# Kernel optimization log

Measured on AMD Instinct MI355X. Metric: run time of the kernel, lower is better.

Reference implementation:

```python
import jax, jax.numpy as jnp
import numpy as np

T, E, IN, OUT, A, R = 16384, 8, 1024, 1024, 8, 16  # tokens, experts, d_in, d_out, adapters, lora rank


def prepare_routing(x, indices, num_groups):
    """Sort tokens by group index; return sorted x, per-group counts, unsort map, sorted ids."""
    sort_idx = jnp.argsort(indices)  # stable sort keeps within-group order
    x_sorted = x[sort_idx]
    group_sizes = jnp.bincount(indices, length=num_groups).astype(jnp.int32)
    unsort_indices = jnp.argsort(sort_idx)
    return x_sorted, group_sizes, unsort_indices, indices[sort_idx]


def setup_inputs() -> dict:
    key = jax.random.key(0)
    ks = jax.random.split(key, 6)
    # tokens pre-sorted by expert: group_sizes must sum to T exactly
    expert_ids = jnp.sort(jax.random.randint(ks[0], (T,), 0, E))
    group_sizes = jnp.bincount(expert_ids, length=E).astype(jnp.int32)
    x = jax.random.normal(ks[1], (T, IN), jnp.float32)
    adapter_indices_sorted = jax.random.randint(ks[2], (T,), 0, A)
    weight = jax.random.normal(ks[3], (E, IN, OUT), jnp.float32) * 0.02
    lora_A = jax.random.normal(ks[4], (A, E, IN, R), jnp.float32) * 0.02
    lora_B = jax.random.normal(ks[5], (A, E, R, OUT), jnp.float32) * 0.02
    lora_scaling = jnp.ones((A,), jnp.float32)
    return {
        "x": x,
        "group_sizes": group_sizes,
        "adapter_indices_sorted": adapter_indices_sorted,
        "weight": weight,
        "lora_A": lora_A,
        "lora_B": lora_B,
        "lora_scaling": lora_scaling,
    }


def reference(x, group_sizes, adapter_indices_sorted, weight, lora_A, lora_B, lora_scaling):
    # base grouped GEMM over experts: [T,IN] x [E,IN,OUT] -> [T,OUT]
    base_out = jax.lax.ragged_dot(x, weight, group_sizes)

    # per-token expert id from contiguous group sizes
    expert_ids = jnp.repeat(jnp.arange(E), group_sizes, total_repeat_length=T)
    flattened = expert_ids * A + adapter_indices_sorted  # expert-major (E,A) group id

    # flatten adapters x experts into E*A groups (expert-major to match flattened ids)
    A_mat = lora_A.transpose(1, 0, 2, 3).reshape(E * A, IN, R)
    B_mat = lora_B.transpose(1, 0, 2, 3).reshape(E * A, R, OUT)

    x_sorted, combined_gs, unsort_indices, _ = prepare_routing(x, flattened, E * A)
    inter = jax.lax.ragged_dot(x_sorted, A_mat, combined_gs)          # [T,R]
    lora_out_sorted = jax.lax.ragged_dot(inter, B_mat, combined_gs)   # [T,OUT]
    lora_out = lora_out_sorted[unsort_indices]
    lora_out = lora_out * lora_scaling[adapter_indices_sorted][:, None]
    return base_out + lora_out
```

## Files before the change

### kernel.cpp

```cpp
#include <hip/hip_runtime.h>

#define T_TOK 16384
#define NEXP 8
#define DIN 1024
#define DOUT 1024
#define NADP 8
#define RANK 16
#define NGRP 64
#define MAXP1 520
#define BK 32
#define NKSTEP 32

typedef float f32x4 __attribute__((ext_vector_type(4)));
typedef float f32x16 __attribute__((ext_vector_type(16)));
typedef __bf16 bf16x8 __attribute__((ext_vector_type(8)));

typedef __attribute__((address_space(3))) void lds_void;
typedef __attribute__((address_space(1))) void g_void;

static __device__ __forceinline__ unsigned short f2bf(float f) {
    union { float f; unsigned u; } c; c.f = f;
    unsigned r = c.u + 0x7FFFu + ((c.u >> 16) & 1u);
    return (unsigned short)(r >> 16);
}

#define XB2 2048
#define NBW 2048
__global__ __launch_bounds__(256) void k_convert_all(const float* __restrict__ x,
                                                     const float* __restrict__ W,
                                                     const float* __restrict__ lA,
                                                     const float* __restrict__ lB,
                                                     unsigned short* __restrict__ xb,
                                                     unsigned short* __restrict__ Wt,
                                                     unsigned short* __restrict__ Agt,
                                                     unsigned short* __restrict__ Blt) {
    __shared__ __attribute__((aligned(16))) unsigned short lds_u[16 * 1032];
    int b = blockIdx.x;
    int t = threadIdx.x;
    if (b < XB2) {
        const size_t total = (size_t)(T_TOK + 128) * DIN / 4;
        const size_t conv  = (size_t)T_TOK * DIN / 4;
        size_t gid = (size_t)b * 256 + t;
#pragma unroll
        for (int it = 0; it < 9; it++) {
            size_t u = gid + (size_t)it * (XB2 * 256);
            if (u < total) {
                ushort4 o;
                if (u < conv) {
                    float4 v = *(const float4*)(x + u * 4);
                    o.x = f2bf(v.x); o.y = f2bf(v.y); o.z = f2bf(v.z); o.w = f2bf(v.w);
                } else {
                    o.x = 0; o.y = 0; o.z = 0; o.w = 0;
                }
                *(ushort4*)(xb + u * 4) = o;
            }
        }
    } else if (b < XB2 + NBW) {
        int idx = b - XB2;
        int e = idx >> 8;
        int k0 = ((idx >> 4) & 15) * 64, n0 = (idx & 15) * 64;
        const float* We = W + (size_t)e * DIN * DOUT;
        unsigned short* Wte = Wt + (size_t)e * DIN * DOUT;
        unsigned* lds32 = (unsigned*)lds_u;
        int kp = t >> 3;
        int nc = (t & 7) * 8;
        const float* r0 = We + (size_t)(k0 + 2 * kp) * DOUT + n0 + nc;
        const float* r1 = r0 + DOUT;
        float4 a0 = *(const float4*)r0, a1 = *(const float4*)(r0 + 4);
        float4 c0 = *(const float4*)r1, c1 = *(const float4*)(r1 + 4);
        lds32[(nc + 0) * 34 + kp] = (unsigned)f2bf(a0.x) | ((unsigned)f2bf(c0.x) << 16);
        lds32[(nc + 1) * 34 + kp] = (unsigned)f2bf(a0.y) | ((unsigned)f2bf(c0.y) << 16);
        lds32[(nc + 2) * 34 + kp] = (unsigned)f2bf(a0.z) | ((unsigned)f2bf(c0.z) << 16);
        lds32[(nc + 3) * 34 + kp] = (unsigned)f2bf(a0.w) | ((unsigned)f2bf(c0.w) << 16);
        lds32[(nc + 4) * 34 + kp] = (unsigned)f2bf(a1.x) | ((unsigned)f2bf(c1.x) << 16);
        lds32[(nc + 5) * 34 + kp] = (unsigned)f2bf(a1.y) | ((unsigned)f2bf(c1.y) << 16);
        lds32[(nc + 6) * 34 + kp] = (unsigned)f2bf(a1.z) | ((unsigned)f2bf(c1.z) << 16);
        lds32[(nc + 7) * 34 + kp] = (unsigned)f2bf(a1.w) | ((unsigned)f2bf(c1.w) << 16);
        __syncthreads();
        int n = t >> 2, kq = (t & 3) * 8;
        uint2 d0 = *(const uint2*)&lds32[n * 34 + kq + 0];
        uint2 d1 = *(const uint2*)&lds32[n * 34 + kq + 2];
        uint2 d2 = *(const uint2*)&lds32[n * 34 + kq + 4];
        uint2 d3 = *(const uint2*)&lds32[n * 34 + kq + 6];
        uint4 v0; v0.x = d0.x; v0.y = d0.y; v0.z = d1.x; v0.w = d1.y;
        uint4 v1; v1.x = d2.x; v1.y = d2.y; v1.z = d3.x; v1.w = d3.y;
        *(uint4*)(Wte + (size_t)(n0 + n) * DIN + k0 + kq * 2) = v0;
        *(uint4*)(Wte + (size_t)(n0 + n) * DIN + k0 + kq * 2 + 8) = v1;
    } else if (b < XB2 + NBW + NGRP) {
        int g = b - (XB2 + NBW);
        int a = g & 7, e = g >> 3;
        const float* src = lA + (size_t)(a * NEXP + e) * DIN * RANK;
#pragma unroll
        for (int it = 0; it < 4; it++) {
            int k = it * 256 + t;
            const float4* p = (const float4*)(src + (size_t)k * RANK);
            float4 v0 = p[0], v1 = p[1], v2 = p[2], v3 = p[3];
            lds_u[0 * 1032 + k] = f2bf(v0.x);  lds_u[1 * 1032 + k] = f2bf(v0.y);
            lds_u[2 * 1032 + k] = f2bf(v0.z);  lds_u[3 * 1032 + k] = f2bf(v0.w);
            lds_u[4 * 1032 + k] = f2bf(v1.x);  lds_u[5 * 1032 + k] = f2bf(v1.y);
            lds_u[6 * 1032 + k] = f2bf(v1.z);  lds_u[7 * 1032 + k] = f2bf(v1.w);
            lds_u[8 * 1032 + k] = f2bf(v2.x);  lds_u[9 * 1032 + k] = f2bf(v2.y);
            lds_u[10 * 1032 + k] = f2bf(v2.z); lds_u[11 * 1032 + k] = f2bf(v2.w);
            lds_u[12 * 1032 + k] = f2bf(v3.x); lds_u[13 * 1032 + k] = f2bf(v3.y);
            lds_u[14 * 1032 + k] = f2bf(v3.z); lds_u[15 * 1032 + k] = f2bf(v3.w);
        }
        __syncthreads();
        unsigned short* dst = Agt + (size_t)g * RANK * DIN;
        int r = t >> 4, ks = (t & 15) * 64;
#pragma unroll
        for (int j = 0; j < 8; j++)
            *(uint4*)(dst + r * DIN + ks + j * 8) = *(const uint4*)&lds_u[r * 1032 + ks + j * 8];
    } else {
        int idx = b - (XB2 + NBW + NGRP);
        int e = idx >> 3, nc = idx & 7;
        int k = t >> 1, half = t & 1;
        int a = k >> 4, r = k & 15;
        const float* src = lB + ((size_t)(a * NEXP + e) * RANK + r) * DOUT + nc * 128 + half * 64;
#pragma unroll
        for (int j = 0; j < 16; j++) {
            float4 v = *(const float4*)(src + j * 4);
            int nl = half * 64 + j * 4;
            lds_u[k * 129 + nl + 0] = f2bf(v.x);
            lds_u[k * 129 + nl + 1] = f2bf(v.y);
            lds_u[k * 129 + nl + 2] = f2bf(v.z);
            lds_u[k * 129 + nl + 3] = f2bf(v.w);
        }
        __syncthreads();
        int nl = t >> 1, kh = t & 1;
        unsigned short* dst = Blt + ((size_t)(e * 1024 + nc * 128 + nl)) * 128 + kh * 64;
#pragma unroll
        for (int g2 = 0; g2 < 8; g2++) {
            uint4 pv;
            unsigned short s0 = lds_u[(kh * 64 + g2 * 8 + 0) * 129 + nl];
            unsigned short s1 = lds_u[(kh * 64 + g2 * 8 + 1) * 129 + nl];
            unsigned short s2 = lds_u[(kh * 64 + g2 * 8 + 2) * 129 + nl];
            unsigned short s3 = lds_u[(kh * 64 + g2 * 8 + 3) * 129 + nl];
            unsigned short s4 = lds_u[(kh * 64 + g2 * 8 + 4) * 129 + nl];
            unsigned short s5 = lds_u[(kh * 64 + g2 * 8 + 5) * 129 + nl];
            unsigned short s6 = lds_u[(kh * 64 + g2 * 8 + 6) * 129 + nl];
            unsigned short s7 = lds_u[(kh * 64 + g2 * 8 + 7) * 129 + nl];
            pv.x = (unsigned)s0 | ((unsigned)s1 << 16);
            pv.y = (unsigned)s2 | ((unsigned)s3 << 16);
            pv.z = (unsigned)s4 | ((unsigned)s5 << 16);
            pv.w = (unsigned)s6 | ((unsigned)s7 << 16);
            *(uint4*)(dst + g2 * 8) = pv;
        }
    }
}

__global__ __launch_bounds__(256) void k_pass1(const unsigned short* __restrict__ xb,
                                               const unsigned short* __restrict__ Agt,
                                               const int* __restrict__ gs,
                                               const int* __restrict__ aidx,
                                               const float* __restrict__ scal,
                                               unsigned short* __restrict__ interb) {
    int bid = blockIdx.x;
    int e = -1, m0 = 0, valid = 0;
    {
        int acc_t = 0, base = 0;
#pragma unroll
        for (int ee = 0; ee < NEXP; ee++) {
            int sz = gs[ee];
            int nt = (sz + 31) >> 5;
            if (e < 0 && bid < acc_t + nt) {
                int loc = bid - acc_t;
                e = ee; m0 = base + (loc << 5);
                int v = sz - (loc << 5); valid = v > 32 ? 32 : v;
            }
            acc_t += nt; base += sz;
        }
    }
    if (e < 0) return;

    int t = threadIdx.x;
    int lane = t & 63, w = t >> 6;
    int ln = lane & 15, q = lane >> 4;

    const unsigned short* A0 = Agt + ((size_t)(e * NADP + 2 * w) * RANK + ln) * DIN + q * 8;
    const unsigned short* A1 = A0 + (size_t)RANK * DIN;
    const unsigned short* X0 = xb + (size_t)(m0 + ln) * DIN + q * 8;

    f32x4 acc[2][2];
#pragma unroll
    for (int i = 0; i < 2; i++) {
        acc[i][0] = (f32x4){0.f, 0.f, 0.f, 0.f};
        acc[i][1] = (f32x4){0.f, 0.f, 0.f, 0.f};
    }

#pragma unroll 4
    for (int k0 = 0; k0 < DIN; k0 += 32) {
        bf16x8 b0 = *(const bf16x8*)(A0 + k0);
        bf16x8 b1 = *(const bf16x8*)(A1 + k0);
#pragma unroll
        for (int rg = 0; rg < 2; rg++) {
            bf16x8 af = *(const bf16x8*)(X0 + (size_t)(rg * 16) * DIN + k0);
            acc[rg][0] = __builtin_amdgcn_mfma_f32_16x16x32_bf16(b0, af, acc[rg][0], 0, 0, 0);
            acc[rg][1] = __builtin_amdgcn_mfma_f32_16x16x32_bf16(b1, af, acc[rg][1], 0, 0, 0);
        }
    }

    float s0 = scal[2 * w], s1 = scal[2 * w + 1];
#pragma unroll
    for (int rg = 0; rg < 2; rg++) {
        int tr = rg * 16 + ln;
        if (tr < valid) {
            int tok = m0 + tr;
            int a = aidx[tok];
            if (a == 2 * w) {
                f32x4 v = acc[rg][0];
                ushort4 u;
                u.x = f2bf(s0 * v[0]); u.y = f2bf(s0 * v[1]);
                u.z = f2bf(s0 * v[2]); u.w = f2bf(s0 * v[3]);
                *(ushort4*)(interb + (size_t)tok * RANK + q * 4) = u;
            } else if (a == 2 * w + 1) {
                f32x4 v = acc[rg][1];
                ushort4 u;
                u.x = f2bf(s1 * v[0]); u.y = f2bf(s1 * v[1]);
                u.z = f2bf(s1 * v[2]); u.w = f2bf(s1 * v[3]);
                *(ushort4*)(interb + (size_t)tok * RANK + q * 4) = u;
            }
        }
    }
}

__global__ __launch_bounds__(256) void k_gemm(const unsigned short* __restrict__ xb,
                                              const unsigned short* __restrict__ wt,
                                              const int* __restrict__ gs,
                                              const unsigned short* __restrict__ interb,
                                              const int* __restrict__ aidx,
                                              const unsigned short* __restrict__ Blt,
                                              float* __restrict__ out) {
    __shared__ __attribute__((aligned(16))) unsigned short smem[32768];

    int id = blockIdx.y * 8 + blockIdx.x;
    int xcd = id & 7;
    int j = id >> 3;
    int tileid = xcd * 17 + (j >> 3);
    int n0 = (j & 7) * 128;

    int e = -1, m0 = 0, valid = 0;
    {
        int acc_t = 0, base = 0;
#pragma unroll
        for (int ee = 0; ee < NEXP; ee++) {
            int sz = gs[ee];
            int nt = (sz + 127) >> 7;
            if (e < 0 && tileid < acc_t + nt) {
                int loc = tileid - acc_t;
                e = ee; m0 = base + (loc << 7);
                int v = sz - (loc << 7); valid = v > 128 ? 128 : v;
            }
            acc_t += nt; base += sz;
        }
    }
    if (e < 0) return;

    int t = threadIdx.x;
    int lane = t & 63;
    int wave = t >> 6;
    int wm = wave >> 1, wn = wave & 1;
    int r32 = lane & 31, hi = lane >> 5;

    const unsigned short* wte = wt + (size_t)e * DIN * DOUT;

    f32x16 acc[2][2];
#pragma unroll
    for (int i = 0; i < 2; i++)
#pragma unroll
        for (int j2 = 0; j2 < 2; j2++) acc[i][j2] = (f32x16)(0.f);

    int srow = wave * 16 + (lane >> 2);
    int skoff = (((lane & 3) ^ ((lane >> 2) ^ (lane >> 4)) ) & 3) * 8;
    const unsigned short* gA = xb + (size_t)m0 * DIN;
    const unsigned short* gB = wte + (size_t)n0 * DIN;

    auto STAGE = [&](int buf, int k0) {
#pragma unroll
        for (int jj = 0; jj < 2; jj++) {
            int row = jj * 64 + srow;
            __builtin_amdgcn_global_load_lds(
                (const g_void*)(gA + (size_t)row * DIN + k0 + skoff),
                (lds_void*)((char*)smem + buf * 16384 + jj * 4096 + wave * 1024), 16, 0, 0);
            __builtin_amdgcn_global_load_lds(
                (const g_void*)(gB + (size_t)row * DIN + k0 + skoff),
                (lds_void*)((char*)smem + buf * 16384 + 8192 + jj * 4096 + wave * 1024), 16, 0, 0);
        }
    };

    int fr = (r32 ^ (r32 >> 2)) & 3;

    auto COMPUTE = [&](int buf) {
        const char* Ab = (const char*)smem + buf * 16384;
        const char* Bb = Ab + 8192;
        __builtin_amdgcn_s_setprio(1);
#pragma unroll
        for (int kf = 0; kf < 2; kf++) {
            int kc = kf * 2 + hi;
            int slot = (kc ^ fr) * 16;
            bf16x8 af[2], bfr[2];
#pragma unroll
            for (int mi = 0; mi < 2; mi++) {
                int row = wm * 64 + mi * 32 + r32;
                af[mi] = *(const bf16x8*)(Ab + row * 64 + slot);
            }
#pragma unroll
            for (int ni = 0; ni < 2; ni++) {
                int row = wn * 64 + ni * 32 + r32;
                bfr[ni] = *(const bf16x8*)(Bb + row * 64 + slot);
            }
#pragma unroll
            for (int mi = 0; mi < 2; mi++)
#pragma unroll
                for (int ni = 0; ni < 2; ni++)
                    acc[mi][ni] = __builtin_amdgcn_mfma_f32_32x32x16_bf16(af[mi], bfr[ni], acc[mi][ni], 0, 0, 0);
        }
        __builtin_amdgcn_s_setprio(0);
    };

    STAGE(0, 0);
    STAGE(1, 32);
    STAGE(2, 64);
#pragma unroll
    for (int ts = 0; ts < NKSTEP; ts++) {
        if (ts < NKSTEP - 2)      asm volatile("s_waitcnt vmcnt(8)" ::: "memory");
        else if (ts == NKSTEP - 2) asm volatile("s_waitcnt vmcnt(4)" ::: "memory");
        else                       asm volatile("s_waitcnt vmcnt(0)" ::: "memory");
        __builtin_amdgcn_s_barrier();
        COMPUTE(ts & 3);
        if (ts < NKSTEP - 3) {
            __builtin_amdgcn_s_barrier();
            STAGE((ts + 3) & 3, (ts + 3) * BK);
        }
    }

    {
        int row = t >> 1, h = t & 1;
        int rs = row & 15;
        uint4 z = {0u, 0u, 0u, 0u};
        uint4 payload = z;
        int pslot = -1;
        if (row < valid) {
            int tok = m0 + row;
            int a = aidx[tok];
            payload = *(const uint4*)(interb + (size_t)tok * RANK + h * 8);
            pslot = a * 2 + h;
        }
#pragma unroll
        for (int l2 = 0; l2 < 8; l2++) {
            int l = l2 * 2 + h;
            int phys = l ^ rs;
            *(uint4*)((char*)smem + row * 256 + phys * 16) = (l == pslot) ? payload : z;
        }
    }
    __syncthreads();
#pragma unroll
    for (int kf = 0; kf < 8; kf++) {
        int kc = kf * 2 + hi;
        bf16x8 af[2], bfr[2];
#pragma unroll
        for (int ni = 0; ni < 2; ni++) {
            int n = wn * 64 + ni * 32 + r32;
            bfr[ni] = *(const bf16x8*)(Blt + ((size_t)(e * 1024 + n0 + n)) * 128 + kc * 8);
        }
#pragma unroll
        for (int mi = 0; mi < 2; mi++) {
            int row = wm * 64 + mi * 32 + r32;
            int slot = kc ^ (r32 & 15);
            af[mi] = *(const bf16x8*)((const char*)smem + row * 256 + slot * 16);
        }
#pragma unroll
        for (int mi = 0; mi < 2; mi++)
#pragma unroll
            for (int ni = 0; ni < 2; ni++)
                acc[mi][ni] = __builtin_amdgcn_mfma_f32_32x32x16_bf16(af[mi], bfr[ni], acc[mi][ni], 0, 0, 0);
    }

#pragma unroll
    for (int mi = 0; mi < 2; mi++) {
#pragma unroll
        for (int r = 0; r < 16; r++) {
            int row32 = (r & 3) + 8 * (r >> 2) + 4 * hi;
            int row_l = wm * 64 + mi * 32 + row32;
            if (row_l < valid) {
                float* orow = out + (size_t)(m0 + row_l) * DOUT + n0 + wn * 64 + r32;
#pragma unroll
                for (int ni = 0; ni < 2; ni++)
                    orow[ni * 32] = acc[mi][ni][r];
            }
        }
    }
}

extern "C" void kernel_launch(void* const* d_in, const int* in_sizes, int n_in,
                              void* d_out, int out_size, void* d_ws, size_t ws_size,
                              hipStream_t stream) {
    (void)in_sizes; (void)n_in; (void)out_size; (void)ws_size;
    const float* x    = (const float*)d_in[0];
    const int*   gs   = (const int*)d_in[1];
    const int*   aidx = (const int*)d_in[2];
    const float* W    = (const float*)d_in[3];
    const float* lA   = (const float*)d_in[4];
    const float* lB   = (const float*)d_in[5];
    const float* scal = (const float*)d_in[6];
    float* out = (float*)d_out;

    char* ws = (char*)d_ws;
    unsigned short* xb     = (unsigned short*)ws;        size_t o = 33816576;
    unsigned short* wt     = (unsigned short*)(ws + o);  o += 16777216;
    unsigned short* Agt    = (unsigned short*)(ws + o);  o += 2097152;
    unsigned short* Blt    = (unsigned short*)(ws + o);  o += 2097152;
    unsigned short* interb = (unsigned short*)(ws + o);  o += 524288;

    k_convert_all<<<XB2 + NBW + NGRP + 64, 256, 0, stream>>>(x, W, lA, lB, xb, wt, Agt, Blt);
    k_pass1<<<MAXP1, 256, 0, stream>>>(xb, Agt, gs, aidx, scal, interb);
    k_gemm<<<dim3(8, 136), 256, 0, stream>>>(xb, wt, gs, interb, aidx, Blt, out);
}
```

Measured before the change: 269.3 us.

## Fuse LoRA-A pass into conversion kernel and halve GEMM barriers per K-step

The LoRA-A projection pass now reads fp32 x directly and converts it on the fly. That lets it run as part of the conversion launch, concurrently with the x/W/B conversions, instead of waiting for the bf16 copy of x. Converting lora_A moves into a small separate kernel that runs first. The main GEMM now processes two 32-wide LDS buffers per iteration (BK 64, 16 steps), which halves the barrier and wait count. The trade-off is extra fp32 reads and conversion work in the LoRA pass, and less prefetch slack in the pipeline.

```diff
diff --git a/kernel.cpp b/kernel.cpp
--- a/kernel.cpp
+++ b/kernel.cpp
@@ -7,9 +7,9 @@
 #define NADP 8
 #define RANK 16
 #define NGRP 64
-#define MAXP1 520
-#define BK 32
-#define NKSTEP 32
+#define NP1 520
+#define BK 64
+#define NKSTEP 16
 
 typedef float f32x4 __attribute__((ext_vector_type(4)));
 typedef float f32x16 __attribute__((ext_vector_type(16)));
@@ -24,23 +24,131 @@
     return (unsigned short)(r >> 16);
 }
 
+__global__ __launch_bounds__(256) void k_prep(const float* __restrict__ lA,
+                                              unsigned short* __restrict__ Agt) {
+    __shared__ __attribute__((aligned(16))) unsigned short lds_u[16 * 1032];
+    int g = blockIdx.x;
+    int t = threadIdx.x;
+    int a = g & 7, e = g >> 3;
+    const float* src = lA + (size_t)(a * NEXP + e) * DIN * RANK;
+#pragma unroll
+    for (int it = 0; it < 4; it++) {
+        int k = it * 256 + t;
+        const float4* p = (const float4*)(src + (size_t)k * RANK);
+        float4 v0 = p[0], v1 = p[1], v2 = p[2], v3 = p[3];
+        lds_u[0 * 1032 + k] = f2bf(v0.x);  lds_u[1 * 1032 + k] = f2bf(v0.y);
+        lds_u[2 * 1032 + k] = f2bf(v0.z);  lds_u[3 * 1032 + k] = f2bf(v0.w);
+        lds_u[4 * 1032 + k] = f2bf(v1.x);  lds_u[5 * 1032 + k] = f2bf(v1.y);
+        lds_u[6 * 1032 + k] = f2bf(v1.z);  lds_u[7 * 1032 + k] = f2bf(v1.w);
+        lds_u[8 * 1032 + k] = f2bf(v2.x);  lds_u[9 * 1032 + k] = f2bf(v2.y);
+        lds_u[10 * 1032 + k] = f2bf(v2.z); lds_u[11 * 1032 + k] = f2bf(v2.w);
+        lds_u[12 * 1032 + k] = f2bf(v3.x); lds_u[13 * 1032 + k] = f2bf(v3.y);
+        lds_u[14 * 1032 + k] = f2bf(v3.z); lds_u[15 * 1032 + k] = f2bf(v3.w);
+    }
+    __syncthreads();
+    unsigned short* dst = Agt + (size_t)g * RANK * DIN;
+    int r = t >> 4, ks = (t & 15) * 64;
+#pragma unroll
+    for (int j = 0; j < 8; j++)
+        *(uint4*)(dst + r * DIN + ks + j * 8) = *(const uint4*)&lds_u[r * 1032 + ks + j * 8];
+}
+
 #define XB2 2048
 #define NBW 2048
-__global__ __launch_bounds__(256) void k_convert_all(const float* __restrict__ x,
-                                                     const float* __restrict__ W,
-                                                     const float* __restrict__ lA,
-                                                     const float* __restrict__ lB,
-                                                     unsigned short* __restrict__ xb,
-                                                     unsigned short* __restrict__ Wt,
-                                                     unsigned short* __restrict__ Agt,
-                                                     unsigned short* __restrict__ Blt) {
+__global__ __launch_bounds__(256) void k_mega(const float* __restrict__ x,
+                                              const float* __restrict__ W,
+                                              const float* __restrict__ lB,
+                                              const unsigned short* __restrict__ Agt,
+                                              const int* __restrict__ gs,
+                                              const int* __restrict__ aidx,
+                                              const float* __restrict__ scal,
+                                              unsigned short* __restrict__ xb,
+                                              unsigned short* __restrict__ Wt,
+                                              unsigned short* __restrict__ Blt,
+                                              unsigned short* __restrict__ interb) {
     __shared__ __attribute__((aligned(16))) unsigned short lds_u[16 * 1032];
     int b = blockIdx.x;
     int t = threadIdx.x;
-    if (b < XB2) {
+    if (b < NP1) {
+        int e = -1, m0 = 0, valid = 0;
+        {
+            int acc_t = 0, base = 0;
+#pragma unroll
+            for (int ee = 0; ee < NEXP; ee++) {
+                int sz = gs[ee];
+                int nt = (sz + 31) >> 5;
+                if (e < 0 && b < acc_t + nt) {
+                    int loc = b - acc_t;
+                    e = ee; m0 = base + (loc << 5);
+                    int v = sz - (loc << 5); valid = v > 32 ? 32 : v;
+                }
+                acc_t += nt; base += sz;
+            }
+        }
+        if (e < 0) return;
+
+        int lane = t & 63, w = t >> 6;
+        int ln = lane & 15, q = lane >> 4;
+
+        const unsigned short* A0 = Agt + ((size_t)(e * NADP + 2 * w) * RANK + ln) * DIN + q * 8;
+        const unsigned short* A1 = A0 + (size_t)RANK * DIN;
+        int r0 = m0 + ln;       if (r0 >= T_TOK) r0 = T_TOK - 1;
+        int r1 = m0 + 16 + ln;  if (r1 >= T_TOK) r1 = T_TOK - 1;
+        const float* X0 = x + (size_t)r0 * DIN + q * 8;
+        const float* X1 = x + (size_t)r1 * DIN + q * 8;
+
+        f32x4 acc[2][2];
+#pragma unroll
+        for (int i = 0; i < 2; i++) {
+            acc[i][0] = (f32x4){0.f, 0.f, 0.f, 0.f};
+            acc[i][1] = (f32x4){0.f, 0.f, 0.f, 0.f};
+        }
+
+#pragma unroll 4
+        for (int k0 = 0; k0 < DIN; k0 += 32) {
+            bf16x8 b0 = *(const bf16x8*)(A0 + k0);
+            bf16x8 b1 = *(const bf16x8*)(A1 + k0);
+#pragma unroll
+            for (int rg = 0; rg < 2; rg++) {
+                const float* xp = (rg == 0) ? (X0 + k0) : (X1 + k0);
+                float4 u0 = *(const float4*)xp;
+                float4 u1 = *(const float4*)(xp + 4);
+                unsigned short af_u[8];
+                af_u[0] = f2bf(u0.x); af_u[1] = f2bf(u0.y); af_u[2] = f2bf(u0.z); af_u[3] = f2bf(u0.w);
+                af_u[4] = f2bf(u1.x); af_u[5] = f2bf(u1.y); af_u[6] = f2bf(u1.z); af_u[7] = f2bf(u1.w);
+                bf16x8 af = *(const bf16x8*)af_u;
+                acc[rg][0] = __builtin_amdgcn_mfma_f32_16x16x32_bf16(b0, af, acc[rg][0], 0, 0, 0);
+                acc[rg][1] = __builtin_amdgcn_mfma_f32_16x16x32_bf16(b1, af, acc[rg][1], 0, 0, 0);
+            }
+        }
+
+        float s0 = scal[2 * w], s1 = scal[2 * w + 1];
+#pragma unroll
+        for (int rg = 0; rg < 2; rg++) {
+            int tr = rg * 16 + ln;
+            if (tr < valid) {
+                int tok = m0 + tr;
+                int a = aidx[tok];
+                if (a == 2 * w) {
+                    f32x4 v = acc[rg][0];
+                    ushort4 u;
+                    u.x = f2bf(s0 * v[0]); u.y = f2bf(s0 * v[1]);
+                    u.z = f2bf(s0 * v[2]); u.w = f2bf(s0 * v[3]);
+                    *(ushort4*)(interb + (size_t)tok * RANK + q * 4) = u;
+                } else if (a == 2 * w + 1) {
+                    f32x4 v = acc[rg][1];
+                    ushort4 u;
+                    u.x = f2bf(s1 * v[0]); u.y = f2bf(s1 * v[1]);
+                    u.z = f2bf(s1 * v[2]); u.w = f2bf(s1 * v[3]);
+                    *(ushort4*)(interb + (size_t)tok * RANK + q * 4) = u;
+                }
+            }
+        }
+    } else if (b < NP1 + XB2) {
+        int bx = b - NP1;
         const size_t total = (size_t)(T_TOK + 128) * DIN / 4;
         const size_t conv  = (size_t)T_TOK * DIN / 4;
-        size_t gid = (size_t)b * 256 + t;
+        size_t gid = (size_t)bx * 256 + t;
 #pragma unroll
         for (int it = 0; it < 9; it++) {
             size_t u = gid + (size_t)it * (XB2 * 256);
@@ -55,8 +163,8 @@
                 *(ushort4*)(xb + u * 4) = o;
             }
         }
-    } else if (b < XB2 + NBW) {
-        int idx = b - XB2;
+    } else if (b < NP1 + XB2 + NBW) {
+        int idx = b - (NP1 + XB2);
         int e = idx >> 8;
         int k0 = ((idx >> 4) & 15) * 64, n0 = (idx & 15) * 64;
         const float* We = W + (size_t)e * DIN * DOUT;
@@ -86,32 +194,8 @@
         uint4 v1; v1.x = d2.x; v1.y = d2.y; v1.z = d3.x; v1.w = d3.y;
         *(uint4*)(Wte + (size_t)(n0 + n) * DIN + k0 + kq * 2) = v0;
         *(uint4*)(Wte + (size_t)(n0 + n) * DIN + k0 + kq * 2 + 8) = v1;
-    } else if (b < XB2 + NBW + NGRP) {
-        int g = b - (XB2 + NBW);
-        int a = g & 7, e = g >> 3;
-        const float* src = lA + (size_t)(a * NEXP + e) * DIN * RANK;
-#pragma unroll
-        for (int it = 0; it < 4; it++) {
-            int k = it * 256 + t;
-            const float4* p = (const float4*)(src + (size_t)k * RANK);
-            float4 v0 = p[0], v1 = p[1], v2 = p[2], v3 = p[3];
-            lds_u[0 * 1032 + k] = f2bf(v0.x);  lds_u[1 * 1032 + k] = f2bf(v0.y);
-            lds_u[2 * 1032 + k] = f2bf(v0.z);  lds_u[3 * 1032 + k] = f2bf(v0.w);
-            lds_u[4 * 1032 + k] = f2bf(v1.x);  lds_u[5 * 1032 + k] = f2bf(v1.y);
-            lds_u[6 * 1032 + k] = f2bf(v1.z);  lds_u[7 * 1032 + k] = f2bf(v1.w);
-            lds_u[8 * 1032 + k] = f2bf(v2.x);  lds_u[9 * 1032 + k] = f2bf(v2.y);
-            lds_u[10 * 1032 + k] = f2bf(v2.z); lds_u[11 * 1032 + k] = f2bf(v2.w);
-            lds_u[12 * 1032 + k] = f2bf(v3.x); lds_u[13 * 1032 + k] = f2bf(v3.y);
-            lds_u[14 * 1032 + k] = f2bf(v3.z); lds_u[15 * 1032 + k] = f2bf(v3.w);
-        }
-        __syncthreads();
-        unsigned short* dst = Agt + (size_t)g * RANK * DIN;
-        int r = t >> 4, ks = (t & 15) * 64;
-#pragma unroll
-        for (int j = 0; j < 8; j++)
-            *(uint4*)(dst + r * DIN + ks + j * 8) = *(const uint4*)&lds_u[r * 1032 + ks + j * 8];
     } else {
-        int idx = b - (XB2 + NBW + NGRP);
+        int idx = b - (NP1 + XB2 + NBW);
         int e = idx >> 3, nc = idx & 7;
         int k = t >> 1, half = t & 1;
         int a = k >> 4, r = k & 15;
@@ -148,81 +232,6 @@
     }
 }
 
-__global__ __launch_bounds__(256) void k_pass1(const unsigned short* __restrict__ xb,
-                                               const unsigned short* __restrict__ Agt,
-                                               const int* __restrict__ gs,
-                                               const int* __restrict__ aidx,
-                                               const float* __restrict__ scal,
-                                               unsigned short* __restrict__ interb) {
-    int bid = blockIdx.x;
-    int e = -1, m0 = 0, valid = 0;
-    {
-        int acc_t = 0, base = 0;
-#pragma unroll
-        for (int ee = 0; ee < NEXP; ee++) {
-            int sz = gs[ee];
-            int nt = (sz + 31) >> 5;
-            if (e < 0 && bid < acc_t + nt) {
-                int loc = bid - acc_t;
-                e = ee; m0 = base + (loc << 5);
-                int v = sz - (loc << 5); valid = v > 32 ? 32 : v;
-            }
-            acc_t += nt; base += sz;
-        }
-    }
-    if (e < 0) return;
-
-    int t = threadIdx.x;
-    int lane = t & 63, w = t >> 6;
-    int ln = lane & 15, q = lane >> 4;
-
-    const unsigned short* A0 = Agt + ((size_t)(e * NADP + 2 * w) * RANK + ln) * DIN + q * 8;
-    const unsigned short* A1 = A0 + (size_t)RANK * DIN;
-    const unsigned short* X0 = xb + (size_t)(m0 + ln) * DIN + q * 8;
-
-    f32x4 acc[2][2];
-#pragma unroll
-    for (int i = 0; i < 2; i++) {
-        acc[i][0] = (f32x4){0.f, 0.f, 0.f, 0.f};
-        acc[i][1] = (f32x4){0.f, 0.f, 0.f, 0.f};
-    }
-
-#pragma unroll 4
-    for (int k0 = 0; k0 < DIN; k0 += 32) {
-        bf16x8 b0 = *(const bf16x8*)(A0 + k0);
-        bf16x8 b1 = *(const bf16x8*)(A1 + k0);
-#pragma unroll
-        for (int rg = 0; rg < 2; rg++) {
-            bf16x8 af = *(const bf16x8*)(X0 + (size_t)(rg * 16) * DIN + k0);
-            acc[rg][0] = __builtin_amdgcn_mfma_f32_16x16x32_bf16(b0, af, acc[rg][0], 0, 0, 0);
-            acc[rg][1] = __builtin_amdgcn_mfma_f32_16x16x32_bf16(b1, af, acc[rg][1], 0, 0, 0);
-        }
-    }
-
-    float s0 = scal[2 * w], s1 = scal[2 * w + 1];
-#pragma unroll
-    for (int rg = 0; rg < 2; rg++) {
-        int tr = rg * 16 + ln;
-        if (tr < valid) {
-            int tok = m0 + tr;
-            int a = aidx[tok];
-            if (a == 2 * w) {
-                f32x4 v = acc[rg][0];
-                ushort4 u;
-                u.x = f2bf(s0 * v[0]); u.y = f2bf(s0 * v[1]);
-                u.z = f2bf(s0 * v[2]); u.w = f2bf(s0 * v[3]);
-                *(ushort4*)(interb + (size_t)tok * RANK + q * 4) = u;
-            } else if (a == 2 * w + 1) {
-                f32x4 v = acc[rg][1];
-                ushort4 u;
-                u.x = f2bf(s1 * v[0]); u.y = f2bf(s1 * v[1]);
-                u.z = f2bf(s1 * v[2]); u.w = f2bf(s1 * v[3]);
-                *(ushort4*)(interb + (size_t)tok * RANK + q * 4) = u;
-            }
-        }
-    }
-}
-
 __global__ __launch_bounds__(256) void k_gemm(const unsigned short* __restrict__ xb,
                                               const unsigned short* __restrict__ wt,
                                               const int* __restrict__ gs,
@@ -270,7 +279,7 @@
         for (int j2 = 0; j2 < 2; j2++) acc[i][j2] = (f32x16)(0.f);
 
     int srow = wave * 16 + (lane >> 2);
-    int skoff = (((lane & 3) ^ ((lane >> 2) ^ (lane >> 4)) ) & 3) * 8;
+    int skoff = (((lane & 3) ^ ((lane >> 2) ^ (lane >> 4))) & 3) * 8;
     const unsigned short* gA = xb + (size_t)m0 * DIN;
     const unsigned short* gB = wte + (size_t)n0 * DIN;
 
@@ -289,10 +298,9 @@
 
     int fr = (r32 ^ (r32 >> 2)) & 3;
 
-    auto COMPUTE = [&](int buf) {
+    auto COMPUTE16 = [&](int buf) {
         const char* Ab = (const char*)smem + buf * 16384;
         const char* Bb = Ab + 8192;
-        __builtin_amdgcn_s_setprio(1);
 #pragma unroll
         for (int kf = 0; kf < 2; kf++) {
             int kc = kf * 2 + hi;
@@ -314,22 +322,24 @@
                 for (int ni = 0; ni < 2; ni++)
                     acc[mi][ni] = __builtin_amdgcn_mfma_f32_32x32x16_bf16(af[mi], bfr[ni], acc[mi][ni], 0, 0, 0);
         }
+    };
+
+    STAGE(0, 0);  STAGE(1, 32);
+    STAGE(2, 64); STAGE(3, 96);
+#pragma unroll
+    for (int ts = 0; ts < NKSTEP; ts++) {
+        if (ts < NKSTEP - 1) asm volatile("s_waitcnt vmcnt(8)" ::: "memory");
+        else                 asm volatile("s_waitcnt vmcnt(0)" ::: "memory");
+        __builtin_amdgcn_s_barrier();
+        int p = ts & 1;
+        __builtin_amdgcn_s_setprio(1);
+        COMPUTE16(2 * p);
+        COMPUTE16(2 * p + 1);
         __builtin_amdgcn_s_setprio(0);
-    };
-
-    STAGE(0, 0);
-    STAGE(1, 32);
-    STAGE(2, 64);
-#pragma unroll
-    for (int ts = 0; ts < NKSTEP; ts++) {
-        if (ts < NKSTEP - 2)      asm volatile("s_waitcnt vmcnt(8)" ::: "memory");
-        else if (ts == NKSTEP - 2) asm volatile("s_waitcnt vmcnt(4)" ::: "memory");
-        else                       asm volatile("s_waitcnt vmcnt(0)" ::: "memory");
-        __builtin_amdgcn_s_barrier();
-        COMPUTE(ts & 3);
-        if (ts < NKSTEP - 3) {
+        if (ts < NKSTEP - 2) {
             __builtin_amdgcn_s_barrier();
-            STAGE((ts + 3) & 3, (ts + 3) * BK);
+            STAGE(2 * p,     (ts + 2) * BK);
+            STAGE(2 * p + 1, (ts + 2) * BK + 32);
         }
     }
 
@@ -411,7 +421,8 @@
     unsigned short* Blt    = (unsigned short*)(ws + o);  o += 2097152;
     unsigned short* interb = (unsigned short*)(ws + o);  o += 524288;
 
-    k_convert_all<<<XB2 + NBW + NGRP + 64, 256, 0, stream>>>(x, W, lA, lB, xb, wt, Agt, Blt);
-    k_pass1<<<MAXP1, 256, 0, stream>>>(xb, Agt, gs, aidx, scal, interb);
+    k_prep<<<NGRP, 256, 0, stream>>>(lA, Agt);
+    k_mega<<<NP1 + XB2 + NBW + 64, 256, 0, stream>>>(x, W, lB, Agt, gs, aidx, scal,
+                                                     xb, wt, Blt, interb);
     k_gemm<<<dim3(8, 136), 256, 0, stream>>>(xb, wt, gs, interb, aidx, Blt, out);
 }
```

Result: no change. 266.4 us (-1.1%).
